# Kernel tuning notes

Measured on AMD Instinct MI355X. Metric: run time of the kernel, lower is better.

The kernel has to match this reference:

```python
import jax, jax.numpy as jnp
import numpy as np

TOP_K = 2
ROUTED_SCALING = 1.0


def setup_inputs() -> dict:
    key = jax.random.key(0)
    k1, k2, k3, k4 = jax.random.split(key, 4)
    S, B, H = 1024, 2, 1024
    E, FFN = 8, 1408
    return {
        "hidden_states": jax.random.normal(k1, (S, B, H), dtype=jnp.float32),
        "gate_w": jax.random.normal(k2, (E, H), dtype=jnp.float32) * 0.02,
        "w1": jax.random.normal(k3, (E, H, 2 * FFN), dtype=jnp.float32) * 0.02,
        "w2": jax.random.normal(k4, (E, FFN, H), dtype=jnp.float32) * 0.02,
    }


def reference(hidden_states, gate_w, w1, w2):
    # hidden_states: [S, B, H] -> transpose(0,1) as in MoELayer.forward
    x = jnp.transpose(hidden_states, (1, 0, 2))  # [B, S, H]
    B, S, H = x.shape
    E = gate_w.shape[0]
    xt = x.reshape(-1, H)  # [T, H], T = B*S
    T = xt.shape[0]

    # --- TopKGate ('greedy', softmax scoring) ---
    scores = jax.nn.softmax(xt @ gate_w.T, axis=-1)  # [T, E]
    topk_w, topk_idx = jax.lax.top_k(scores, TOP_K)  # [T, K]
    # norm_topk_prob: normalize the top-k weights
    topk_w = topk_w / (jnp.sum(topk_w, axis=-1, keepdims=True) + 1e-20)
    topk_w = topk_w * ROUTED_SCALING

    # Sparse combine weights [T, E] (zero for non-selected experts)
    combine = jnp.zeros((T, E), dtype=xt.dtype)
    combine = combine.at[jnp.arange(T)[:, None], topk_idx].set(topk_w)

    # --- Experts: per-expert swiglu MLP, weighted combine ---
    # Equivalent math to dispatch -> per-expert grouped GEMM -> combine:
    # non-selected experts contribute with weight 0.
    out = jnp.zeros_like(xt)
    for e in range(E):
        h = xt @ w1[e]                      # [T, 2*FFN]
        g, u = jnp.split(h, 2, axis=-1)
        y = (jax.nn.silu(g) * u) @ w2[e]    # [T, H]
        out = out + combine[:, e:e + 1] * y

    out = out.reshape(B, S, H)
    return jnp.transpose(out, (1, 0, 2))  # back to [S, B, H]
```

## Files before the change

### kernel.cpp

```cpp
#include <hip/hip_runtime.h>
#include <hip/hip_bf16.h>

#define S_      1024
#define B_      2
#define H_      1024
#define E_      8
#define FFN_    1408
#define TWO_FFN 2816
#define T_      2048
#define MAXSLOTS 5120
#define MAXTILES 40

typedef float  f32x4 __attribute__((ext_vector_type(4)));
typedef short  s16x8 __attribute__((ext_vector_type(8)));

__device__ __forceinline__ unsigned short f2bf(float f) {
    unsigned u = __float_as_uint(f);
    u += 0x7fffu + ((u >> 16) & 1u);
    return (unsigned short)(u >> 16);
}
__device__ __forceinline__ float bf2f(unsigned short h) {
    return __uint_as_float(((unsigned)h) << 16);
}
__device__ __forceinline__ void async16(const void* g, void* l) {
    __builtin_amdgcn_global_load_lds(
        (const __attribute__((address_space(1))) unsigned int*)(unsigned long long)g,
        (__attribute__((address_space(3))) unsigned int*)(unsigned long long)l,
        16, 0, 0);
}
__device__ __forceinline__ size_t xrow_off(int t) {
    return (size_t)(t & (S_ - 1)) * (B_ * H_) + (size_t)(t >> 10) * H_;
}

__global__ void k_convert_gate(const float* __restrict__ hs, const float* __restrict__ gw,
                               unsigned short* __restrict__ xb,
                               int* __restrict__ topkI, float* __restrict__ topkW,
                               int* __restrict__ ctrl) {
    int wid = threadIdx.x >> 6, lane = threadIdx.x & 63;
    int t = blockIdx.x * 4 + wid;
    const float* xr = hs + xrow_off(t);
    unsigned short* xo = xb + (size_t)t * H_;
    float acc[E_];
#pragma unroll
    for (int e = 0; e < E_; e++) acc[e] = 0.f;
#pragma unroll
    for (int p = 0; p < 4; p++) {
        int h = p * 256 + lane * 4;
        const float4 v = *(const float4*)(xr + h);
        unsigned short o[4] = { f2bf(v.x), f2bf(v.y), f2bf(v.z), f2bf(v.w) };
        *(uint2*)(xo + h) = *(const uint2*)o;
#pragma unroll
        for (int e = 0; e < E_; e++) {
            const float4 g = *(const float4*)(gw + e * H_ + h);
            acc[e] += v.x * g.x + v.y * g.y + v.z * g.z + v.w * g.w;
        }
    }
#pragma unroll
    for (int e = 0; e < E_; e++)
        for (int off = 32; off > 0; off >>= 1) acc[e] += __shfl_down(acc[e], off);
    if (lane == 0) {
        float l0 = -1e30f, l1 = -1e30f; int i0 = 0, i1 = 0;
#pragma unroll
        for (int e = 0; e < E_; e++) {
            float v = acc[e];
            if (v > l0)      { l1 = l0; i1 = i0; l0 = v; i0 = e; }
            else if (v > l1) { l1 = v;  i1 = e; }
        }
        float p1 = expf(l1 - l0);
        float w0 = 1.f / (1.f + p1);
        float w1 = 1.f - w0;
        topkI[2 * t] = i0; topkI[2 * t + 1] = i1;
        topkW[2 * t] = w0; topkW[2 * t + 1] = w1;
        atomicAdd(&ctrl[i0], 1);
        atomicAdd(&ctrl[i1], 1);
    }
}

__global__ void k_transpose_bf16(const float* __restrict__ in, unsigned short* __restrict__ out,
                                 int R, int C) {
    __shared__ float tile[32][33];
    int e = blockIdx.z;
    const float* ip = in + (size_t)e * R * C;
    unsigned short* op = out + (size_t)e * R * C;
    int c0 = blockIdx.x * 32, r0 = blockIdx.y * 32;
    int tx = threadIdx.x, ty = threadIdx.y;
#pragma unroll
    for (int i = 0; i < 4; i++)
        tile[ty + i * 8][tx] = ip[(size_t)(r0 + ty + i * 8) * C + c0 + tx];
    __syncthreads();
#pragma unroll
    for (int i = 0; i < 4; i++)
        op[(size_t)(c0 + ty + i * 8) * R + r0 + tx] = f2bf(tile[tx][ty + i * 8]);
}

__global__ void k_routeassign(const int* __restrict__ topkI, const float* __restrict__ topkW,
                              int* __restrict__ ctrl, int* __restrict__ perm,
                              float* __restrict__ wgt, int* __restrict__ slotOfTok) {
    __shared__ int s_base[E_];
    __shared__ int s_cur[E_];
    int tid = threadIdx.x;
    if (tid == 0) {
        int cnt[E_];
#pragma unroll
        for (int e = 0; e < E_; e++) cnt[e] = ctrl[e];
        int b = 0, nt = 0;
        for (int e = 0; e < E_; e++) {
            s_base[e] = b;
            int ntile = (cnt[e] + 127) >> 7;
            for (int ti = 0; ti < ntile; ti++) { ctrl[32 + nt] = e; ctrl[96 + nt] = b + ti * 128; nt++; }
            b += ntile * 128;
        }
        ctrl[24] = nt;
#pragma unroll
        for (int e = 0; e < E_; e++) s_cur[e] = 0;
    }
    __syncthreads();
    for (int s = tid; s < MAXSLOTS; s += 256) { perm[s] = 0; wgt[s] = 0.f; }
    __syncthreads();
    for (int t = tid; t < T_; t += 256) {
#pragma unroll
        for (int k = 0; k < 2; k++) {
            int e = topkI[2 * t + k];
            int pos = atomicAdd(&s_cur[e], 1);
            int slot = s_base[e] + pos;
            perm[slot] = t;
            wgt[slot]  = topkW[2 * t + k];
            slotOfTok[2 * t + k] = slot;
        }
    }
}

__global__ __launch_bounds__(256) void k_gemm1(
    const unsigned short* __restrict__ xb, const unsigned short* __restrict__ w1bt,
    const int* __restrict__ ctrl, const int* __restrict__ perm,
    unsigned short* __restrict__ C1) {
    int nt = ctrl[24];
    int tileIdx = blockIdx.x;
    if (tileIdx >= nt) return;
    int e     = ctrl[32 + tileIdx];
    int slot0 = ctrl[96 + tileIdx];
    int ct    = blockIdx.y;
    __shared__ unsigned short As[128 * 64];
    __shared__ unsigned short Bs[128 * 64];
    int tid = threadIdx.x, wid = tid >> 6, lane = tid & 63;

    const unsigned short* aPtr[4];
    const unsigned short* bPtr[4];
    unsigned short* lA[4];
    unsigned short* lB[4];
#pragma unroll
    for (int i = 0; i < 4; i++) {
        int c = (wid * 4 + i) * 64 + lane;
        int r = c >> 3;
        int qd = (c & 7) ^ (r & 7);
        int col8 = qd * 8;
        int tok = perm[slot0 + r];
        aPtr[i] = xb + (size_t)tok * H_ + col8;
        bPtr[i] = w1bt + ((size_t)e * TWO_FFN + ct * 128 + r) * H_ + col8;
        lA[i] = As + (size_t)c * 8;
        lB[i] = Bs + (size_t)c * 8;
    }
    f32x4 acc[4][4];
#pragma unroll
    for (int mi = 0; mi < 4; mi++)
#pragma unroll
        for (int ni = 0; ni < 4; ni++) acc[mi][ni] = (f32x4){0.f, 0.f, 0.f, 0.f};
    int wm = wid & 1, wn = wid >> 1;
    int rowB = wm * 64, colB = wn * 64;
    int sw = (lane & 7) << 3;

    for (int k0 = 0; k0 < H_; k0 += 64) {
#pragma unroll
        for (int i = 0; i < 4; i++) { async16(aPtr[i] + k0, lA[i]); async16(bPtr[i] + k0, lB[i]); }
        __syncthreads();
#pragma unroll
        for (int kk = 0; kk < 64; kk += 32) {
            int kr = (kk + ((lane >> 4) << 3)) ^ sw;
            s16x8 af[4], bf[4];
#pragma unroll
            for (int mi = 0; mi < 4; mi++) af[mi] = *(const s16x8*)&As[(rowB + mi * 16 + (lane & 15)) * 64 + kr];
#pragma unroll
            for (int ni = 0; ni < 4; ni++) bf[ni] = *(const s16x8*)&Bs[(colB + ni * 16 + (lane & 15)) * 64 + kr];
#pragma unroll
            for (int mi = 0; mi < 4; mi++)
#pragma unroll
                for (int ni = 0; ni < 4; ni++)
                    acc[mi][ni] = __builtin_amdgcn_mfma_f32_16x16x32_bf16(af[mi], bf[ni], acc[mi][ni], 0, 0, 0);
        }
        __syncthreads();
    }
#pragma unroll
    for (int mi = 0; mi < 4; mi++)
#pragma unroll
        for (int ni = 0; ni < 4; ni++)
#pragma unroll
            for (int r = 0; r < 4; r++) {
                int m = rowB + mi * 16 + (lane >> 4) * 4 + r;
                int n = colB + ni * 16 + (lane & 15);
                C1[(size_t)(slot0 + m) * TWO_FFN + ct * 128 + n] = f2bf(acc[mi][ni][r]);
            }
}

__global__ void k_swiglu(const unsigned short* __restrict__ C1, unsigned short* __restrict__ A2) {
    int gid = blockIdx.x * 256 + threadIdx.x;
    int row = gid / 352;
    int j   = (gid - row * 352) * 4;
    const unsigned short* g = C1 + (size_t)row * TWO_FFN + j;
    unsigned short o[4];
#pragma unroll
    for (int i = 0; i < 4; i++) {
        float gv = bf2f(g[i]);
        float uv = bf2f(g[i + FFN_]);
        float s = gv / (1.f + expf(-gv));
        o[i] = f2bf(s * uv);
    }
    *(uint2*)(A2 + (size_t)row * FFN_ + j) = *(const uint2*)o;
}

__global__ __launch_bounds__(256) void k_gemm2(
    const unsigned short* __restrict__ A2, const unsigned short* __restrict__ w2bt,
    const int* __restrict__ ctrl, float* __restrict__ Yp) {
    int nt = ctrl[24];
    int tileIdx = blockIdx.x;
    if (tileIdx >= nt) return;
    int e     = ctrl[32 + tileIdx];
    int slot0 = ctrl[96 + tileIdx];
    int ct    = blockIdx.y;
    int ks    = blockIdx.z;
    __shared__ unsigned short As[128 * 64];
    __shared__ unsigned short Bs[128 * 64];
    int tid = threadIdx.x, wid = tid >> 6, lane = tid & 63;

    const unsigned short* aPtr[4];
    const unsigned short* bPtr[4];
    unsigned short* lA[4];
    unsigned short* lB[4];
#pragma unroll
    for (int i = 0; i < 4; i++) {
        int c = (wid * 4 + i) * 64 + lane;
        int r = c >> 3;
        int qd = (c & 7) ^ (r & 7);
        int col8 = qd * 8;
        aPtr[i] = A2 + (size_t)(slot0 + r) * FFN_ + col8;
        bPtr[i] = w2bt + ((size_t)e * H_ + ct * 128 + r) * FFN_ + col8;
        lA[i] = As + (size_t)c * 8;
        lB[i] = Bs + (size_t)c * 8;
    }
    f32x4 acc[4][4];
#pragma unroll
    for (int mi = 0; mi < 4; mi++)
#pragma unroll
        for (int ni = 0; ni < 4; ni++) acc[mi][ni] = (f32x4){0.f, 0.f, 0.f, 0.f};
    int wm = wid & 1, wn = wid >> 1;
    int rowB = wm * 64, colB = wn * 64;
    int sw = (lane & 7) << 3;

    int kbeg = ks * (FFN_ / 2), kend = kbeg + FFN_ / 2;
    for (int k0 = kbeg; k0 < kend; k0 += 64) {
#pragma unroll
        for (int i = 0; i < 4; i++) { async16(aPtr[i] + k0, lA[i]); async16(bPtr[i] + k0, lB[i]); }
        __syncthreads();
#pragma unroll
        for (int kk = 0; kk < 64; kk += 32) {
            int kr = (kk + ((lane >> 4) << 3)) ^ sw;
            s16x8 af[4], bf[4];
#pragma unroll
            for (int mi = 0; mi < 4; mi++) af[mi] = *(const s16x8*)&As[(rowB + mi * 16 + (lane & 15)) * 64 + kr];
#pragma unroll
            for (int ni = 0; ni < 4; ni++) bf[ni] = *(const s16x8*)&Bs[(colB + ni * 16 + (lane & 15)) * 64 + kr];
#pragma unroll
            for (int mi = 0; mi < 4; mi++)
#pragma unroll
                for (int ni = 0; ni < 4; ni++)
                    acc[mi][ni] = __builtin_amdgcn_mfma_f32_16x16x32_bf16(af[mi], bf[ni], acc[mi][ni], 0, 0, 0);
        }
        __syncthreads();
    }
    float* yp = Yp + (size_t)ks * MAXSLOTS * H_;
#pragma unroll
    for (int mi = 0; mi < 4; mi++)
#pragma unroll
        for (int r = 0; r < 4; r++) {
            int m = rowB + mi * 16 + (lane >> 4) * 4 + r;
#pragma unroll
            for (int ni = 0; ni < 4; ni++) {
                int n = colB + ni * 16 + (lane & 15);
                yp[(size_t)(slot0 + m) * H_ + ct * 128 + n] = acc[mi][ni][r];
            }
        }
}

__global__ void k_combine(const float* __restrict__ Yp, const int* __restrict__ slotOfTok,
                          const float* __restrict__ topkW, float* __restrict__ out) {
    int t = blockIdx.x;
    int h = threadIdx.x * 4;
    int sA = slotOfTok[2 * t], sB = slotOfTok[2 * t + 1];
    float wA = topkW[2 * t],   wB = topkW[2 * t + 1];
    const float4 a0 = *(const float4*)(Yp + (size_t)sA * H_ + h);
    const float4 a1 = *(const float4*)(Yp + ((size_t)MAXSLOTS + sA) * H_ + h);
    const float4 b0 = *(const float4*)(Yp + (size_t)sB * H_ + h);
    const float4 b1 = *(const float4*)(Yp + ((size_t)MAXSLOTS + sB) * H_ + h);
    float4 r;
    r.x = wA * (a0.x + a1.x) + wB * (b0.x + b1.x);
    r.y = wA * (a0.y + a1.y) + wB * (b0.y + b1.y);
    r.z = wA * (a0.z + a1.z) + wB * (b0.z + b1.z);
    r.w = wA * (a0.w + a1.w) + wB * (b0.w + b1.w);
    *(float4*)(out + xrow_off(t) + h) = r;
}

extern "C" void kernel_launch(void* const* d_in, const int* in_sizes, int n_in,
                              void* d_out, int out_size, void* d_ws, size_t ws_size,
                              hipStream_t stream) {
    (void)in_sizes; (void)n_in; (void)ws_size; (void)out_size;
    const float* hs = (const float*)d_in[0];
    const float* gw = (const float*)d_in[1];
    const float* w1 = (const float*)d_in[2];
    const float* w2 = (const float*)d_in[3];
    float* out = (float*)d_out;
    char* ws = (char*)d_ws;

    int*            ctrl   = (int*)ws;
    int*            topkI  = (int*)(ws + (16u << 10));
    float*          topkW  = (float*)(ws + (48u << 10));
    int*            perm   = (int*)(ws + (80u << 10));
    float*          wgt    = (float*)(ws + (112u << 10));
    int*            slotOfTok = (int*)(ws + (144u << 10));
    unsigned short* xb    = (unsigned short*)(ws + (1ull  << 20));
    unsigned short* w1bt  = (unsigned short*)(ws + (5ull  << 20));
    float*          Yp    = (float*)(ws + (5ull << 20));
    unsigned short* w2bt  = (unsigned short*)(ws + (49ull << 20));
    unsigned short* C1    = (unsigned short*)(ws + (71ull << 20));
    unsigned short* A2    = (unsigned short*)(ws + (99ull << 20));

    hipMemsetAsync(ctrl, 0, 1024, stream);

    k_convert_gate<<<512, 256, 0, stream>>>(hs, gw, xb, topkI, topkW, ctrl);
    k_transpose_bf16<<<dim3(TWO_FFN / 32, H_ / 32, E_), dim3(32, 8), 0, stream>>>(w1, w1bt, H_, TWO_FFN);
    k_transpose_bf16<<<dim3(H_ / 32, FFN_ / 32, E_), dim3(32, 8), 0, stream>>>(w2, w2bt, FFN_, H_);
    k_routeassign<<<1, 256, 0, stream>>>(topkI, topkW, ctrl, perm, wgt, slotOfTok);
    k_gemm1<<<dim3(MAXTILES, TWO_FFN / 128), 256, 0, stream>>>(xb, w1bt, ctrl, perm, C1);
    k_swiglu<<<7040, 256, 0, stream>>>(C1, A2);
    k_gemm2<<<dim3(MAXTILES, H_ / 128, 2), 256, 0, stream>>>(A2, w2bt, ctrl, Yp);
    k_combine<<<2048, 256, 0, stream>>>(Yp, slotOfTok, topkW, out);
}
```

Before: 334.5 us.

## Fuse SwiGLU into gemm1 epilogue, count experts in routeassign, widen transpose tiles

gemm1 now loads matching gate and up columns into the same 128-wide B tile. It passes the up half through LDS and writes the SwiGLU product straight to A2, so the C1 buffer and the separate swiglu kernel go away. Expert counts are now computed inside the single-block routeassign kernel rather than with global atomics in the gate kernel, which also drops the memset. The weight transpose uses 64x64 tiles with 256 threads. The costs are extra LDS traffic in the gemm1 epilogue and a larger shared tile in the transpose.

```diff
diff --git a/kernel.cpp b/kernel.cpp
--- a/kernel.cpp
+++ b/kernel.cpp
@@ -19,9 +19,6 @@
     u += 0x7fffu + ((u >> 16) & 1u);
     return (unsigned short)(u >> 16);
 }
-__device__ __forceinline__ float bf2f(unsigned short h) {
-    return __uint_as_float(((unsigned)h) << 16);
-}
 __device__ __forceinline__ void async16(const void* g, void* l) {
     __builtin_amdgcn_global_load_lds(
         (const __attribute__((address_space(1))) unsigned int*)(unsigned long long)g,
@@ -34,8 +31,7 @@
 
 __global__ void k_convert_gate(const float* __restrict__ hs, const float* __restrict__ gw,
                                unsigned short* __restrict__ xb,
-                               int* __restrict__ topkI, float* __restrict__ topkW,
-                               int* __restrict__ ctrl) {
+                               int* __restrict__ topkI, float* __restrict__ topkW) {
     int wid = threadIdx.x >> 6, lane = threadIdx.x & 63;
     int t = blockIdx.x * 4 + wid;
     const float* xr = hs + xrow_off(t);
@@ -71,42 +67,59 @@
         float w1 = 1.f - w0;
         topkI[2 * t] = i0; topkI[2 * t + 1] = i1;
         topkW[2 * t] = w0; topkW[2 * t + 1] = w1;
-        atomicAdd(&ctrl[i0], 1);
-        atomicAdd(&ctrl[i1], 1);
     }
 }
 
 __global__ void k_transpose_bf16(const float* __restrict__ in, unsigned short* __restrict__ out,
                                  int R, int C) {
-    __shared__ float tile[32][33];
+    __shared__ float tile[64][65];
     int e = blockIdx.z;
     const float* ip = in + (size_t)e * R * C;
     unsigned short* op = out + (size_t)e * R * C;
-    int c0 = blockIdx.x * 32, r0 = blockIdx.y * 32;
+    int c0 = blockIdx.x * 64, r0 = blockIdx.y * 64;
     int tx = threadIdx.x, ty = threadIdx.y;
 #pragma unroll
-    for (int i = 0; i < 4; i++)
-        tile[ty + i * 8][tx] = ip[(size_t)(r0 + ty + i * 8) * C + c0 + tx];
-    __syncthreads();
-#pragma unroll
-    for (int i = 0; i < 4; i++)
-        op[(size_t)(c0 + ty + i * 8) * R + r0 + tx] = f2bf(tile[tx][ty + i * 8]);
+    for (int i = 0; i < 16; i++) {
+        int r = ty + i * 4;
+        tile[tx][r] = ip[(size_t)(r0 + r) * C + c0 + tx];
+    }
+    __syncthreads();
+#pragma unroll
+    for (int i = 0; i < 16; i++) {
+        int c = ty + i * 4;
+        op[(size_t)(c0 + c) * R + r0 + tx] = f2bf(tile[c][tx]);
+    }
 }
 
 __global__ void k_routeassign(const int* __restrict__ topkI, const float* __restrict__ topkW,
                               int* __restrict__ ctrl, int* __restrict__ perm,
                               float* __restrict__ wgt, int* __restrict__ slotOfTok) {
+    __shared__ int s_wcnt[4][E_];
     __shared__ int s_base[E_];
     __shared__ int s_cur[E_];
-    int tid = threadIdx.x;
+    int tid = threadIdx.x, wid = tid >> 6, lane = tid & 63;
+    int cnt[E_];
+#pragma unroll
+    for (int j = 0; j < E_; j++) cnt[j] = 0;
+    for (int i = tid; i < 2 * T_; i += 256) {
+        int e = topkI[i];
+#pragma unroll
+        for (int j = 0; j < E_; j++) cnt[j] += (e == j);
+    }
+#pragma unroll
+    for (int j = 0; j < E_; j++)
+        for (int off = 32; off > 0; off >>= 1) cnt[j] += __shfl_down(cnt[j], off);
+    if (lane == 0) {
+#pragma unroll
+        for (int j = 0; j < E_; j++) s_wcnt[wid][j] = cnt[j];
+    }
+    __syncthreads();
     if (tid == 0) {
-        int cnt[E_];
-#pragma unroll
-        for (int e = 0; e < E_; e++) cnt[e] = ctrl[e];
         int b = 0, nt = 0;
         for (int e = 0; e < E_; e++) {
+            int n = s_wcnt[0][e] + s_wcnt[1][e] + s_wcnt[2][e] + s_wcnt[3][e];
             s_base[e] = b;
-            int ntile = (cnt[e] + 127) >> 7;
+            int ntile = (n + 127) >> 7;
             for (int ti = 0; ti < ntile; ti++) { ctrl[32 + nt] = e; ctrl[96 + nt] = b + ti * 128; nt++; }
             b += ntile * 128;
         }
@@ -133,15 +146,16 @@
 __global__ __launch_bounds__(256) void k_gemm1(
     const unsigned short* __restrict__ xb, const unsigned short* __restrict__ w1bt,
     const int* __restrict__ ctrl, const int* __restrict__ perm,
-    unsigned short* __restrict__ C1) {
+    unsigned short* __restrict__ A2) {
     int nt = ctrl[24];
     int tileIdx = blockIdx.x;
     if (tileIdx >= nt) return;
     int e     = ctrl[32 + tileIdx];
     int slot0 = ctrl[96 + tileIdx];
     int ct    = blockIdx.y;
-    __shared__ unsigned short As[128 * 64];
-    __shared__ unsigned short Bs[128 * 64];
+    __shared__ __align__(16) unsigned short smem[2 * 128 * 64];
+    unsigned short* As = smem;
+    unsigned short* Bs = smem + 128 * 64;
     int tid = threadIdx.x, wid = tid >> 6, lane = tid & 63;
 
     const unsigned short* aPtr[4];
@@ -155,8 +169,9 @@
         int qd = (c & 7) ^ (r & 7);
         int col8 = qd * 8;
         int tok = perm[slot0 + r];
+        int gr = (r < 64) ? (ct * 64 + r) : (FFN_ + ct * 64 + (r - 64));
         aPtr[i] = xb + (size_t)tok * H_ + col8;
-        bPtr[i] = w1bt + ((size_t)e * TWO_FFN + ct * 128 + r) * H_ + col8;
+        bPtr[i] = w1bt + ((size_t)e * TWO_FFN + gr) * H_ + col8;
         lA[i] = As + (size_t)c * 8;
         lB[i] = Bs + (size_t)c * 8;
     }
@@ -189,32 +204,37 @@
         }
         __syncthreads();
     }
-#pragma unroll
-    for (int mi = 0; mi < 4; mi++)
-#pragma unroll
-        for (int ni = 0; ni < 4; ni++)
+    float* upLds = (float*)smem;
+    if (wn == 1) {
+#pragma unroll
+        for (int mi = 0; mi < 4; mi++)
+#pragma unroll
+            for (int ni = 0; ni < 4; ni++)
+#pragma unroll
+                for (int r = 0; r < 4; r++) {
+                    int m = rowB + mi * 16 + (lane >> 4) * 4 + r;
+                    int u = ni * 16 + (lane & 15);
+                    upLds[m * 64 + u] = acc[mi][ni][r];
+                }
+    }
+    __syncthreads();
+    if (wn == 0) {
+#pragma unroll
+        for (int mi = 0; mi < 4; mi++)
 #pragma unroll
             for (int r = 0; r < 4; r++) {
                 int m = rowB + mi * 16 + (lane >> 4) * 4 + r;
-                int n = colB + ni * 16 + (lane & 15);
-                C1[(size_t)(slot0 + m) * TWO_FFN + ct * 128 + n] = f2bf(acc[mi][ni][r]);
+                unsigned short* arow = A2 + (size_t)(slot0 + m) * FFN_ + ct * 64;
+#pragma unroll
+                for (int ni = 0; ni < 4; ni++) {
+                    int gl = ni * 16 + (lane & 15);
+                    float g = acc[mi][ni][r];
+                    float u = upLds[m * 64 + gl];
+                    float s = g / (1.f + expf(-g));
+                    arow[gl] = f2bf(s * u);
+                }
             }
-}
-
-__global__ void k_swiglu(const unsigned short* __restrict__ C1, unsigned short* __restrict__ A2) {
-    int gid = blockIdx.x * 256 + threadIdx.x;
-    int row = gid / 352;
-    int j   = (gid - row * 352) * 4;
-    const unsigned short* g = C1 + (size_t)row * TWO_FFN + j;
-    unsigned short o[4];
-#pragma unroll
-    for (int i = 0; i < 4; i++) {
-        float gv = bf2f(g[i]);
-        float uv = bf2f(g[i + FFN_]);
-        float s = gv / (1.f + expf(-gv));
-        o[i] = f2bf(s * uv);
-    }
-    *(uint2*)(A2 + (size_t)row * FFN_ + j) = *(const uint2*)o;
+    }
 }
 
 __global__ __launch_bounds__(256) void k_gemm2(
@@ -227,8 +247,8 @@
     int slot0 = ctrl[96 + tileIdx];
     int ct    = blockIdx.y;
     int ks    = blockIdx.z;
-    __shared__ unsigned short As[128 * 64];
-    __shared__ unsigned short Bs[128 * 64];
+    __shared__ __align__(16) unsigned short As[128 * 64];
+    __shared__ __align__(16) unsigned short Bs[128 * 64];
     int tid = threadIdx.x, wid = tid >> 6, lane = tid & 63;
 
     const unsigned short* aPtr[4];
@@ -329,17 +349,13 @@
     unsigned short* w1bt  = (unsigned short*)(ws + (5ull  << 20));
     float*          Yp    = (float*)(ws + (5ull << 20));
     unsigned short* w2bt  = (unsigned short*)(ws + (49ull << 20));
-    unsigned short* C1    = (unsigned short*)(ws + (71ull << 20));
-    unsigned short* A2    = (unsigned short*)(ws + (99ull << 20));
-
-    hipMemsetAsync(ctrl, 0, 1024, stream);
-
-    k_convert_gate<<<512, 256, 0, stream>>>(hs, gw, xb, topkI, topkW, ctrl);
-    k_transpose_bf16<<<dim3(TWO_FFN / 32, H_ / 32, E_), dim3(32, 8), 0, stream>>>(w1, w1bt, H_, TWO_FFN);
-    k_transpose_bf16<<<dim3(H_ / 32, FFN_ / 32, E_), dim3(32, 8), 0, stream>>>(w2, w2bt, FFN_, H_);
+    unsigned short* A2    = (unsigned short*)(ws + (71ull << 20));
+
+    k_convert_gate<<<512, 256, 0, stream>>>(hs, gw, xb, topkI, topkW);
+    k_transpose_bf16<<<dim3(TWO_FFN / 64, H_ / 64, E_), dim3(64, 4), 0, stream>>>(w1, w1bt, H_, TWO_FFN);
+    k_transpose_bf16<<<dim3(H_ / 64, FFN_ / 64, E_), dim3(64, 4), 0, stream>>>(w2, w2bt, FFN_, H_);
     k_routeassign<<<1, 256, 0, stream>>>(topkI, topkW, ctrl, perm, wgt, slotOfTok);
-    k_gemm1<<<dim3(MAXTILES, TWO_FFN / 128), 256, 0, stream>>>(xb, w1bt, ctrl, perm, C1);
-    k_swiglu<<<7040, 256, 0, stream>>>(C1, A2);
+    k_gemm1<<<dim3(MAXTILES, FFN_ / 64), 256, 0, stream>>>(xb, w1bt, ctrl, perm, A2);
     k_gemm2<<<dim3(MAXTILES, H_ / 128, 2), 256, 0, stream>>>(A2, w2bt, ctrl, Yp);
     k_combine<<<2048, 256, 0, stream>>>(Yp, slotOfTok, topkW, out);
 }
```

New measurement: 289.8 us. -13.4%, faster.
